# Performance work log

Measured on AMD Instinct MI355X. Metric: run time of the kernel, lower is better.

## Reference

```python
import jax, jax.numpy as jnp
import numpy as np

NUM_CLASSES = 5
OVERLAP = 0.5
THRESH = 0.3


def _decode(loc, defaults):
    # loc: [N,2] (center offset, log-width offset); defaults: [N,2] (center, width)
    c = defaults[:, 0] + loc[:, 0] * defaults[:, 1]
    w = defaults[:, 1] * jnp.exp(loc[:, 1])
    return jnp.stack([c - 0.5 * w, c + 0.5 * w], axis=1)  # [N,2] start/end


def _nms_keep(boxes, scores, valid, overlap):
    # boxes [N,2], scores [N], valid [N] bool -> keep mask [N] bool (original order)
    N = scores.shape[0]
    masked = jnp.where(valid, scores, -jnp.inf)
    order = jnp.argsort(-masked)               # descending by score
    b = boxes[order]
    v = valid[order]
    start, end = b[:, 0], b[:, 1]
    length = end - start
    inter = jnp.clip(jnp.minimum(end[:, None], end[None, :]) -
                     jnp.maximum(start[:, None], start[None, :]), 0.0)
    union = length[:, None] + length[None, :] - inter
    iou = inter / jnp.maximum(union, 1e-12)
    idx = jnp.arange(N)
    # suppress_mat[i,j]: j is lower-ranked than i and overlaps i above threshold
    suppress_mat = (iou > overlap) & (idx[None, :] > idx[:, None])

    def body(i, keep):
        sup = keep[i] & suppress_mat[i]
        return keep & ~sup

    keep_sorted = jax.lax.fori_loop(0, N, body, v)
    return jnp.zeros((N,), bool).at[order].set(keep_sorted)


def setup_inputs() -> dict:
    key = jax.random.key(0)
    k1, k2, k3, k4 = jax.random.split(key, 4)
    B, N, C = 8, 2048, NUM_CLASSES
    localizations = 0.5 * jax.random.normal(k1, (B, N, 2), dtype=jnp.float32)
    classifications = 2.0 * jax.random.normal(k2, (B, N, C), dtype=jnp.float32)
    centers = jax.random.uniform(k3, (N, 1), dtype=jnp.float32)               # in [0,1]
    widths = 0.01 + 0.05 * jax.random.uniform(k4, (N, 1), dtype=jnp.float32)  # positive
    localizations_default = jnp.concatenate([centers, widths], axis=1)
    return {"localizations": localizations,
            "classifications": classifications,
            "localizations_default": localizations_default}


def reference(localizations, classifications, localizations_default):
    # softmax over classes
    scores = jax.nn.softmax(classifications, axis=2)             # [B,N,C]
    decoded = jax.vmap(_decode, in_axes=(0, None))(localizations, localizations_default)  # [B,N,2]
    cls_scores = jnp.transpose(scores[:, :, 1:], (0, 2, 1))      # [B,C-1,N] (skip background)
    valid = cls_scores > THRESH                                  # per-class threshold filter

    nms_per_class = jax.vmap(lambda s, v, bx: _nms_keep(bx, s, v, OVERLAP),
                             in_axes=(0, 0, None))               # over classes
    keep = jax.vmap(nms_per_class, in_axes=(0, 0, 0))(cls_scores, valid, decoded)  # [B,C-1,N]

    # final sanity filter: start > -10 and end < 10
    in_range = (decoded[:, :, 0] > -10.0) & (decoded[:, :, 1] < 10.0)  # [B,N]
    keep = keep & in_range[:, None, :]

    # dense output: (start, end, score) per kept event, zeros elsewhere -> [B,C-1,N,3]
    boxes_bc = jnp.broadcast_to(decoded[:, None, :, :], keep.shape + (2,))
    out = jnp.concatenate([boxes_bc, cls_scores[..., None]], axis=-1)
    return out * keep[..., None].astype(out.dtype)
```

## Files before the change

### kernel.cpp

```cpp
#include <hip/hip_runtime.h>
#include <math.h>

#define N_ANCHORS 2048
#define THRESH 0.3f
#define OVERLAP 0.5f
#define NBC 32
#define BLOCK 1024
#define NW 16


__global__ __launch_bounds__(BLOCK, 1) void det_mono(
    const float* __restrict__ loc, const float* __restrict__ cls,
    const float* __restrict__ defs, float* __restrict__ out)
{
#pragma clang fp contract(off)
    const int tid  = threadIdx.x;
    const int lane = tid & 63;
    const int wid  = tid >> 6;
    const int bc   = blockIdx.x;
    const int b    = bc >> 2;
    const int c    = bc & 3;

    __shared__ __align__(16) float          csc[2052];
    __shared__ __align__(16) float2         cbx[2048];
    __shared__                unsigned short cid[2048];
    __shared__ __align__(16) float2         sbox[2048];
    __shared__                float          ssc[2048];
    __shared__                unsigned short sid[2048];
    __shared__ __align__(16) float4         kbx[2048];
    __shared__ unsigned long long diag[64];
    __shared__ unsigned long long deadp[NW];
    __shared__ unsigned long long keptg[32];
    __shared__ int s_rp[512];
    __shared__ int s_wsum[NW], s_woff[NW], s_V, s_K;

    float* const outb = out + (size_t)bc * N_ANCHORS * 3;
    {
        float4 z4 = make_float4(0.f, 0.f, 0.f, 0.f);
        float4* ob4 = (float4*)outb;
#pragma unroll 1
        for (int i = tid; i < (N_ANCHORS * 3) / 4; i += BLOCK) ob4[i] = z4;
    }
    if (tid < 32) keptg[tid] = 0ull;
    if (tid == 0) s_K = 0;

    const int base = tid * 2;
    float c10[10], l4v[4], d4v[4];
    {
        const float2* cp2 = (const float2*)(cls + ((size_t)b * N_ANCHORS + base) * 5);
#pragma unroll
        for (int q = 0; q < 5; ++q) ((float2*)c10)[q] = cp2[q];
        ((float4*)l4v)[0] = *(const float4*)(loc + ((size_t)b * N_ANCHORS + base) * 2);
        ((float4*)d4v)[0] = *(const float4*)(defs + (size_t)base * 2);
    }
    float sc2[2], bs2[2], be2[2];
    int vmask = 0, cnt = 0;
#pragma unroll
    for (int k = 0; k < 2; ++k) {
        float x0 = c10[5*k+0], x1 = c10[5*k+1], x2 = c10[5*k+2],
              x3 = c10[5*k+3], x4 = c10[5*k+4];
        float m  = fmaxf(fmaxf(fmaxf(fmaxf(x0, x1), x2), x3), x4);
        float e0 = expf(x0 - m), e1 = expf(x1 - m), e2 = expf(x2 - m),
              e3 = expf(x3 - m), e4 = expf(x4 - m);
        float sum = e0 + e1 + e2 + e3 + e4;
        float ec  = (c == 0) ? e1 : (c == 1) ? e2 : (c == 2) ? e3 : e4;
        float score = ec / sum;
        float l0 = l4v[2*k], l1 = l4v[2*k+1];
        float d0 = d4v[2*k], d1 = d4v[2*k+1];
        float cc = d0 + l0 * d1;
        float w  = d1 * expf(l1);
        sc2[k] = score;
        bs2[k] = cc - 0.5f * w;
        be2[k] = cc + 0.5f * w;
        if (score > THRESH) { vmask |= (1 << k); cnt++; }
    }

    int inc = cnt;
#pragma unroll
    for (int d = 1; d < 64; d <<= 1) {
        int v = __shfl_up(inc, d);
        if (lane >= d) inc += v;
    }
    if (lane == 63) s_wsum[wid] = inc;
    __syncthreads();
    if (tid == 0) {
        int o = 0;
        for (int w = 0; w < NW; ++w) { s_woff[w] = o; o += s_wsum[w]; }
        s_V = o;
    }
    __syncthreads();
    {
        int off = s_woff[wid] + (inc - cnt);
#pragma unroll
        for (int k = 0; k < 2; ++k) {
            if (vmask & (1 << k)) {
                csc[off] = sc2[k];
                cbx[off] = make_float2(bs2[k], be2[k]);
                cid[off] = (unsigned short)(base + k);
                off++;
            }
        }
    }
    __syncthreads();
    const int V = s_V;
    const int W = (V + 63) >> 6;
    const int SCend = W << 6;
    if (tid < 4) csc[V + tid] = -INFINITY;
    __syncthreads();

    {
        const float4* cs4 = (const float4*)csc;
        const int n4 = (V + 3) >> 2;
        if (V <= 512) {
            const int p  = tid & 511;
            const int sg = tid >> 9;
            const int h4 = n4 >> 1;
            const int i40 = sg ? h4 : 0, i41 = sg ? n4 : h4;
            int r = 0; float s = 0.f;
            if (p < V) {
                s = csc[p];
#pragma unroll 2
                for (int i4 = i40; i4 < i41; ++i4) {
                    float4 s4 = cs4[i4];
                    int ib = i4 << 2;
                    r += (s4.x > s || (s4.x == s && ib     < p)) ? 1 : 0;
                    r += (s4.y > s || (s4.y == s && ib + 1 < p)) ? 1 : 0;
                    r += (s4.z > s || (s4.z == s && ib + 2 < p)) ? 1 : 0;
                    r += (s4.w > s || (s4.w == s && ib + 3 < p)) ? 1 : 0;
                }
            }
            if (sg && p < V) s_rp[p] = r;
            __syncthreads();
            if (!sg && p < V) {
                r += s_rp[p];
                sbox[r] = cbx[p];
                ssc[r]  = s;
                sid[r]  = cid[p];
            }
        } else {
#pragma unroll 1
            for (int p = tid; p < V; p += BLOCK) {
                float s = csc[p];
                int r = 0;
#pragma unroll 2
                for (int i4 = 0; i4 < n4; ++i4) {
                    float4 s4 = cs4[i4];
                    int ib = i4 << 2;
                    r += (s4.x > s || (s4.x == s && ib     < p)) ? 1 : 0;
                    r += (s4.y > s || (s4.y == s && ib + 1 < p)) ? 1 : 0;
                    r += (s4.z > s || (s4.z == s && ib + 2 < p)) ? 1 : 0;
                    r += (s4.w > s || (s4.w == s && ib + 3 < p)) ? 1 : 0;
                }
                sbox[r] = cbx[p];
                ssc[r]  = s;
                sid[r]  = cid[p];
            }
        }
    }
#pragma unroll 1
    for (int i = V + tid; i < SCend; i += BLOCK)
        sbox[i] = make_float2(1e30f, 1e30f);
    __syncthreads();

#pragma unroll 1
    for (int g = 0; g < W; ++g) {
        const int u = (g << 6) + lane;
        const float2 cb = sbox[u];
        const float  cl = cb.y - cb.x;

        const int K = s_K;
        bool dead = false;
#pragma unroll 1
        for (int i = wid; i < K; i += NW) {
            float4 kb = kbx[i];
            float in = fmaxf(fminf(cb.y, kb.y) - fmaxf(cb.x, kb.x), 0.0f);
            float un = kb.z + cl - in;
            dead |= (in > OVERLAP * fmaxf(un, 1e-12f));
        }
        {
            unsigned long long db = __ballot(dead);
            if (lane == 0) deadp[wid] = db;
        }

#pragma unroll
        for (int q = 0; q < 4; ++q) {
            const int r = (wid << 2) + q;
            const float2 rb = sbox[(g << 6) + r];
            const float  rl = rb.y - rb.x;
            float in = fmaxf(fminf(rb.y, cb.y) - fmaxf(rb.x, cb.x), 0.0f);
            float un = cl + rl - in;
            bool sup = (in > OVERLAP * fmaxf(un, 1e-12f));
            unsigned long long bal = __ballot(sup);
            if (lane == 0) diag[r] = bal & ((1ull << r) - 1ull);
        }
        __syncthreads();

        if (wid == 0) {
            unsigned long long dw = 0ull;
#pragma unroll
            for (int i = 0; i < NW; ++i) dw |= deadp[i];
            const unsigned long long rself = diag[lane];
            int rem = V - (g << 6);
            unsigned long long valid = (rem >= 64) ? ~0ull : ((1ull << rem) - 1ull);
            unsigned long long cand = valid & ~dw;
            unsigned long long kw = 0ull;
            while (cand) {
                unsigned long long suppw = __ballot((rself & cand) != 0ull);
                unsigned long long nk = cand & ~suppw;
                if (!nk) nk = cand & (~cand + 1ull);
                kw |= nk;
                unsigned long long ddw = __ballot((rself & nk) != 0ull);
                cand &= ~(nk | ddw);
            }
            if ((kw >> lane) & 1ull) {
                int pos = s_K + __popcll(kw & ((1ull << lane) - 1ull));
                kbx[pos] = make_float4(cb.x, cb.y, cl, 0.f);
            }
            if (lane == 0) { keptg[g] = kw; s_K += __popcll(kw); }
        }
        __syncthreads();
    }

#pragma unroll 1
    for (int r = tid; r < V; r += BLOCK) {
        if ((keptg[r >> 6] >> (r & 63)) & 1ull) {
            float2 bx = sbox[r];
            if (bx.x > -10.0f && bx.y < 10.0f) {
                int n = sid[r];
                float* o = outb + (size_t)n * 3;
                o[0] = bx.x;
                o[1] = bx.y;
                o[2] = ssc[r];
            }
        }
    }
}

extern "C" void kernel_launch(void* const* d_in, const int* in_sizes, int n_in,
                              void* d_out, int out_size, void* d_ws, size_t ws_size,
                              hipStream_t stream) {
    const float* loc  = (const float*)d_in[0];
    const float* cls  = (const float*)d_in[1];
    const float* defs = (const float*)d_in[2];
    float* out = (float*)d_out;
    (void)d_ws; (void)ws_size;
    det_mono<<<NBC, BLOCK, 0, stream>>>(loc, cls, defs, out);
}
```

Measured before the change: 91.63 us.

## Replace quadratic rank sort with float-bit bucket sort and ballot compaction

The all-pairs rank computation used to sort valid scores is replaced by a histogram over the high bits of each score's float pattern, which are guaranteed to lie in (0.3, 1]. A 64-lane scan turns the histogram into descending bucket offsets, atomics scatter indices into buckets, and each element is then ranked only against the members of its own bucket. The warp prefix sum used for stream compaction is also swapped for ballot plus popcount. This cuts the sort work from quadratic to near-linear, at the cost of shared-memory atomics and reliance on the threshold-derived bucket base.

```diff
diff --git a/kernel.cpp b/kernel.cpp
--- a/kernel.cpp
+++ b/kernel.cpp
@@ -7,6 +7,7 @@
 #define NBC 32
 #define BLOCK 1024
 #define NW 16
+#define BUCKET_BASE 32051
 
 
 __global__ __launch_bounds__(BLOCK, 1) void det_mono(
@@ -21,17 +22,19 @@
     const int b    = bc >> 2;
     const int c    = bc & 3;
 
-    __shared__ __align__(16) float          csc[2052];
+    __shared__ __align__(16) float          csc[2048];
     __shared__ __align__(16) float2         cbx[2048];
     __shared__                unsigned short cid[2048];
     __shared__ __align__(16) float2         sbox[2048];
     __shared__                float          ssc[2048];
     __shared__                unsigned short sid[2048];
     __shared__ __align__(16) float4         kbx[2048];
+    __shared__                unsigned short blist[2048];
+    __shared__ int s_hist[512];
+    __shared__ int s_off[512];
     __shared__ unsigned long long diag[64];
     __shared__ unsigned long long deadp[NW];
     __shared__ unsigned long long keptg[32];
-    __shared__ int s_rp[512];
     __shared__ int s_wsum[NW], s_woff[NW], s_V, s_K;
 
     float* const outb = out + (size_t)bc * N_ANCHORS * 3;
@@ -42,6 +45,7 @@
         for (int i = tid; i < (N_ANCHORS * 3) / 4; i += BLOCK) ob4[i] = z4;
     }
     if (tid < 32) keptg[tid] = 0ull;
+    if (tid < 512) s_hist[tid] = 0;
     if (tid == 0) s_K = 0;
 
     const int base = tid * 2;
@@ -54,7 +58,7 @@
         ((float4*)d4v)[0] = *(const float4*)(defs + (size_t)base * 2);
     }
     float sc2[2], bs2[2], be2[2];
-    int vmask = 0, cnt = 0;
+    int vmask = 0;
 #pragma unroll
     for (int k = 0; k < 2; ++k) {
         float x0 = c10[5*k+0], x1 = c10[5*k+1], x2 = c10[5*k+2],
@@ -72,16 +76,14 @@
         sc2[k] = score;
         bs2[k] = cc - 0.5f * w;
         be2[k] = cc + 0.5f * w;
-        if (score > THRESH) { vmask |= (1 << k); cnt++; }
-    }
-
-    int inc = cnt;
-#pragma unroll
-    for (int d = 1; d < 64; d <<= 1) {
-        int v = __shfl_up(inc, d);
-        if (lane >= d) inc += v;
-    }
-    if (lane == 63) s_wsum[wid] = inc;
+        if (score > THRESH) vmask |= (1 << k);
+    }
+
+    const unsigned long long lmlt = (1ull << lane) - 1ull;
+    unsigned long long b0 = __ballot(vmask & 1);
+    unsigned long long b1 = __ballot(vmask & 2);
+    int exc  = __popcll(b0 & lmlt) + __popcll(b1 & lmlt);
+    if (lane == 0) s_wsum[wid] = __popcll(b0) + __popcll(b1);
     __syncthreads();
     if (tid == 0) {
         int o = 0;
@@ -90,7 +92,7 @@
     }
     __syncthreads();
     {
-        int off = s_woff[wid] + (inc - cnt);
+        int off = s_woff[wid] + exc;
 #pragma unroll
         for (int k = 0; k < 2; ++k) {
             if (vmask & (1 << k)) {
@@ -105,57 +107,52 @@
     const int V = s_V;
     const int W = (V + 63) >> 6;
     const int SCend = W << 6;
-    if (tid < 4) csc[V + tid] = -INFINITY;
-    __syncthreads();
-
-    {
-        const float4* cs4 = (const float4*)csc;
-        const int n4 = (V + 3) >> 2;
-        if (V <= 512) {
-            const int p  = tid & 511;
-            const int sg = tid >> 9;
-            const int h4 = n4 >> 1;
-            const int i40 = sg ? h4 : 0, i41 = sg ? n4 : h4;
-            int r = 0; float s = 0.f;
-            if (p < V) {
-                s = csc[p];
-#pragma unroll 2
-                for (int i4 = i40; i4 < i41; ++i4) {
-                    float4 s4 = cs4[i4];
-                    int ib = i4 << 2;
-                    r += (s4.x > s || (s4.x == s && ib     < p)) ? 1 : 0;
-                    r += (s4.y > s || (s4.y == s && ib + 1 < p)) ? 1 : 0;
-                    r += (s4.z > s || (s4.z == s && ib + 2 < p)) ? 1 : 0;
-                    r += (s4.w > s || (s4.w == s && ib + 3 < p)) ? 1 : 0;
-                }
-            }
-            if (sg && p < V) s_rp[p] = r;
-            __syncthreads();
-            if (!sg && p < V) {
-                r += s_rp[p];
-                sbox[r] = cbx[p];
-                ssc[r]  = s;
-                sid[r]  = cid[p];
-            }
-        } else {
-#pragma unroll 1
-            for (int p = tid; p < V; p += BLOCK) {
-                float s = csc[p];
-                int r = 0;
-#pragma unroll 2
-                for (int i4 = 0; i4 < n4; ++i4) {
-                    float4 s4 = cs4[i4];
-                    int ib = i4 << 2;
-                    r += (s4.x > s || (s4.x == s && ib     < p)) ? 1 : 0;
-                    r += (s4.y > s || (s4.y == s && ib + 1 < p)) ? 1 : 0;
-                    r += (s4.z > s || (s4.z == s && ib + 2 < p)) ? 1 : 0;
-                    r += (s4.w > s || (s4.w == s && ib + 3 < p)) ? 1 : 0;
-                }
-                sbox[r] = cbx[p];
-                ssc[r]  = s;
-                sid[r]  = cid[p];
-            }
-        }
+
+#pragma unroll 1
+    for (int p = tid; p < V; p += BLOCK) {
+        unsigned bkt = (__float_as_uint(csc[p]) >> 15) - BUCKET_BASE;
+        atomicAdd(&s_hist[bkt], 1);
+    }
+    __syncthreads();
+    if (wid == 0) {
+        int running = 0;
+#pragma unroll 1
+        for (int ch = 0; ch < 8; ++ch) {
+            int bidx = 511 - ((ch << 6) + lane);
+            int v = s_hist[bidx];
+            int incv = v;
+#pragma unroll
+            for (int d = 1; d < 64; d <<= 1) {
+                int t = __shfl_up(incv, d);
+                if (lane >= d) incv += t;
+            }
+            s_off[bidx] = running + incv - v;
+            running += __shfl(incv, 63);
+        }
+    }
+    __syncthreads();
+#pragma unroll 1
+    for (int p = tid; p < V; p += BLOCK) {
+        unsigned bkt = (__float_as_uint(csc[p]) >> 15) - BUCKET_BASE;
+        int slot = atomicAdd(&s_off[bkt], 1);
+        blist[slot] = (unsigned short)p;
+    }
+    __syncthreads();
+#pragma unroll 1
+    for (int p = tid; p < V; p += BLOCK) {
+        float s = csc[p];
+        unsigned bkt = (__float_as_uint(s) >> 15) - BUCKET_BASE;
+        int end = s_off[bkt], cnt = s_hist[bkt];
+        int r = end - cnt;
+#pragma unroll 1
+        for (int t = end - cnt; t < end; ++t) {
+            int e = blist[t];
+            float s2 = csc[e];
+            r += (s2 > s || (s2 == s && e < p)) ? 1 : 0;
+        }
+        sbox[r] = cbx[p];
+        ssc[r]  = s;
+        sid[r]  = cid[p];
     }
 #pragma unroll 1
     for (int i = V + tid; i < SCend; i += BLOCK)
```

Result: faster. 77.87 us (-15.0%).
